# Kernel optimization log

Measured on AMD Instinct MI355X. Metric: run time of the kernel, lower is better.

Reference implementation:

```python
import jax, jax.numpy as jnp
import numpy as np

HEADS = 8
CPH = 32


def _rel_pos_indices(h, w):
    # same construction as the torch buffer, done statically in numpy
    coords = np.stack(np.meshgrid(np.arange(h), np.arange(w), indexing='ij')).reshape(2, -1)  # [2, N]
    rel = coords[:, :, None] - coords[:, None, :]  # [2, N, N]
    idx = (rel[0] + h - 1) * (2 * w - 1) + (rel[1] + w - 1)  # [N, N]
    return jnp.asarray(idx, dtype=jnp.int32)


def setup_inputs() -> dict:
    key = jax.random.key(0)
    ks = jax.random.split(key, 6)
    B, C, H, W = 2, 256, 48, 48
    emb = HEADS * CPH  # 256
    x = jax.random.normal(ks[0], (B, C, H, W), dtype=jnp.float32)
    # GDN params (kept positive so sqrt is well-defined)
    gdn_beta = jnp.ones((C,), dtype=jnp.float32)
    gdn_gamma = 0.1 * jnp.eye(C, dtype=jnp.float32) + 0.001 * jax.random.uniform(ks[1], (C, C), dtype=jnp.float32)
    w_qkv = 0.02 * jax.random.normal(ks[2], (3 * emb, C), dtype=jnp.float32)
    w_out = 0.02 * jax.random.normal(ks[3], (C, emb), dtype=jnp.float32)
    b_out = jnp.zeros((C,), dtype=jnp.float32)
    table_size = (2 * H - 1) * (2 * W - 1)
    rel_bias_table = 0.02 * jax.random.normal(ks[4], (table_size, HEADS), dtype=jnp.float32)
    return {"x": x, "gdn_beta": gdn_beta, "gdn_gamma": gdn_gamma,
            "w_qkv": w_qkv, "w_out": w_out, "b_out": b_out,
            "rel_bias_table": rel_bias_table}


def reference(x, gdn_beta, gdn_gamma, w_qkv, w_out, b_out, rel_bias_table):
    B, C, H, W = x.shape
    N = H * W
    emb = HEADS * CPH
    scale = CPH ** (-0.5)

    # GDN: y = x / sqrt(beta + gamma * x^2)  (1x1 conv over channels of x^2)
    norm = jnp.einsum('bchw,dc->bdhw', x * x, gdn_gamma) + gdn_beta[None, :, None, None]
    xn = x / jnp.sqrt(norm)

    # flatten spatial, channels last: [B, N, C]
    t = xn.reshape(B, C, N).transpose(0, 2, 1)

    # qkv projection (no bias)
    qkv = (t @ w_qkv.T).reshape(B, N, 3, HEADS, CPH).transpose(2, 0, 3, 1, 4)  # [3, B, h, N, d]
    q, k, v = qkv[0], qkv[1], qkv[2]

    attn = jnp.einsum('bhnd,bhmd->bhnm', q, k) * scale  # [B, h, N, N]

    # gathered relative position bias: [h, N, N]
    idx = _rel_pos_indices(H, W)  # [N, N], static ints
    bias = rel_bias_table[idx.reshape(-1)].reshape(N, N, HEADS).transpose(2, 0, 1)
    attn = jax.nn.softmax(attn + bias[None], axis=-1)

    # NOTE: faithful to the original quirk — reshape (B, h, N, d) directly
    # to (B, N, C) with NO head/seq transpose, exactly like the torch code.
    res = jnp.einsum('bhnm,bhmd->bhnd', attn, v).reshape(B, N, emb)

    out = res @ w_out.T + b_out  # [B, N, C]
    return out.transpose(0, 2, 1).reshape(B, C, H, W)
```

## Files before the change

kernel.cpp:

```cpp
#include <hip/hip_runtime.h>
#include <cstdint>
#include <cstddef>

typedef __attribute__((ext_vector_type(8))) short short8;
typedef __attribute__((ext_vector_type(4))) float floatx4;

#define NB 2
#define NPIX 2304
#define TBL 9025
#define TBLP 9032
#define L2E 1.4426950408889634f
#define QSCALE 0.17677669529663689f
#define NTILES 36

__device__ __forceinline__ float b2f(unsigned short u) {
  union { unsigned int i; float f; } v; v.i = ((unsigned int)u) << 16; return v.f;
}
__device__ __forceinline__ unsigned short f2b(float f) {
  union { float f; unsigned int i; } v; v.f = f;
  return (unsigned short)((v.i + 0x7fffu + ((v.i >> 16) & 1u)) >> 16);
}
__device__ __forceinline__ unsigned int cvtpk(float lo, float hi) {
  unsigned int r;
  asm("v_cvt_pk_bf16_f32 %0, %1, %2" : "=v"(r) : "v"(lo), "v"(hi));
  return r;
}

__global__ __launch_bounds__(256) void prep_k(
    const float* __restrict__ gamma, const float* __restrict__ wqkv,
    const float* __restrict__ wout, const float* __restrict__ table,
    const float* __restrict__ x,
    unsigned short* __restrict__ gb, unsigned short* __restrict__ qb,
    unsigned short* __restrict__ wb, unsigned short* __restrict__ tb,
    unsigned short* __restrict__ xsq)
{
  __shared__ unsigned short Ls[64][66];
  const int bx = blockIdx.x;
  const int tid = threadIdx.x;
  if (bx < 768) {
    int i = bx * 256 + tid;
    if (i < 65536)  gb[i] = f2b(gamma[i]);
    qb[i] = f2b(wqkv[i]);
    if (i < 65536)  wb[i] = f2b(wout[i]);
    if (i < TBL * 8) {
      int e = i >> 3, h = i & 7;
      tb[(size_t)h * TBLP + e] = f2b(table[i] * L2E);
    }
    return;
  }
  const int t = bx - 768;
  const int b = t / 144, r = t % 144;
  const int c0 = (r / 36) * 64, n0 = (r % 36) * 64;
  {
    const int ci = tid >> 2, ng = (tid & 3) * 16;
    const float* xr = &x[((size_t)(b * 256 + c0 + ci)) * NPIX + n0 + ng];
    unsigned int* dst = (unsigned int*)&Ls[ci][ng];
    #pragma unroll
    for (int j = 0; j < 4; ++j) {
      float4 v = *(const float4*)(xr + j * 4);
      dst[j * 2]     = cvtpk(v.x * v.x, v.y * v.y);
      dst[j * 2 + 1] = cvtpk(v.z * v.z, v.w * v.w);
    }
  }
  __syncthreads();
  {
    const int nr = tid >> 2, cc = (tid & 3) * 16;
    unsigned short* orow = &xsq[((size_t)(b * NPIX) + n0 + nr) * 256 + c0 + cc];
    unsigned short tmp[16];
    #pragma unroll
    for (int j = 0; j < 16; ++j) tmp[j] = Ls[cc + j][nr];
    *(short8*)&orow[0] = *(short8*)&tmp[0];
    *(short8*)&orow[8] = *(short8*)&tmp[8];
  }
}

template<int MODE>
__global__ __launch_bounds__(256) void gemm_k(
    const unsigned short* __restrict__ A,
    const unsigned short* __restrict__ Bw,
    const float* __restrict__ vec,
    const float* __restrict__ X,
    unsigned short* __restrict__ o0,
    unsigned short* __restrict__ o1,
    unsigned short* __restrict__ o2,
    float* __restrict__ of)
{
  const int n0 = blockIdx.x * 64;
  const int m0 = blockIdx.y * 64;
  const int b  = blockIdx.z;
  const int tid = threadIdx.x;
  const int wave = tid >> 6, lane = tid & 63;
  const int wm = wave >> 1, wn = wave & 1;
  const int lm = lane & 15, quad = lane >> 4;

  const unsigned short* pa = &A[(size_t)(m0 + wm * 32 + lm) * 256 + quad * 8];
  const unsigned short* pb = &Bw[((size_t)b * NPIX + n0 + wn * 32 + lm) * 256 + quad * 8];

  floatx4 acc[2][2] = {};
  #pragma unroll
  for (int k0 = 0; k0 < 256; k0 += 32) {
    short8 af0 = *(const short8*)(pa + k0);
    short8 af1 = *(const short8*)(pa + 16 * 256 + k0);
    short8 bf0 = *(const short8*)(pb + k0);
    short8 bf1 = *(const short8*)(pb + 16 * 256 + k0);
    acc[0][0] = __builtin_amdgcn_mfma_f32_16x16x32_bf16(af0, bf0, acc[0][0], 0, 0, 0);
    acc[0][1] = __builtin_amdgcn_mfma_f32_16x16x32_bf16(af0, bf1, acc[0][1], 0, 0, 0);
    acc[1][0] = __builtin_amdgcn_mfma_f32_16x16x32_bf16(af1, bf0, acc[1][0], 0, 0, 0);
    acc[1][1] = __builtin_amdgcn_mfma_f32_16x16x32_bf16(af1, bf1, acc[1][1], 0, 0, 0);
  }

  #pragma unroll
  for (int tm = 0; tm < 2; ++tm) {
    const int rbase = m0 + wm * 32 + tm * 16 + quad * 4;
    #pragma unroll
    for (int tn = 0; tn < 2; ++tn) {
      const int col = n0 + wn * 32 + tn * 16 + lm;
      floatx4 a4 = acc[tm][tn];
      if (MODE == 0) {
        float xn[4];
        #pragma unroll
        for (int r = 0; r < 4; ++r) {
          int d = rbase + r;
          float xv = X[((size_t)(b * 256 + d)) * NPIX + col];
          xn[r] = xv * rsqrtf(vec[d] + a4[r]);
        }
        uint2 pk = { cvtpk(xn[0], xn[1]), cvtpk(xn[2], xn[3]) };
        *(uint2*)&o0[((size_t)(b * NPIX + col)) * 256 + rbase] = pk;
      } else if (MODE == 1) {
        const int part = rbase >> 8, h = (rbase >> 5) & 7, dd = rbase & 31;
        if (part == 2) {
          #pragma unroll
          for (int r = 0; r < 4; ++r)
            o2[(((size_t)(b * 8 + h)) * 32 + dd + r) * NPIX + col] = f2b(a4[r]);
        } else {
          unsigned short* dst = part == 0 ? o0 : o1;
          const float sc = (part == 0) ? (QSCALE * L2E) : 1.0f;
          uint2 pk = { cvtpk(a4[0] * sc, a4[1] * sc), cvtpk(a4[2] * sc, a4[3] * sc) };
          *(uint2*)&dst[(((size_t)(b * 8 + h)) * NPIX + col) * 32 + dd] = pk;
        }
      } else {
        #pragma unroll
        for (int r = 0; r < 4; ++r) {
          int c = rbase + r;
          of[((size_t)(b * 256 + c)) * NPIX + col] = a4[r] + vec[c];
        }
      }
    }
  }
}

__global__ __launch_bounds__(576) void attn_k(
    const unsigned short* __restrict__ qg, const unsigned short* __restrict__ kg,
    const unsigned short* __restrict__ vt, const unsigned short* __restrict__ tabt,
    unsigned short* __restrict__ ob)
{
  __shared__ __align__(16) unsigned short tab[TBLP];
  __shared__ __align__(16) unsigned short Pl[9][16][72];

  const int tid = threadIdx.x;
  const int w = tid >> 6, lane = tid & 63;
  const int lm = lane & 15, quad = lane >> 4;
  const int bh = blockIdx.x;
  const int q0 = blockIdx.y * 144;
  const size_t base = (size_t)bh * NPIX * 32;

  {
    const unsigned short* src = tabt + (size_t)(bh & 7) * TBLP;
    for (int e = tid * 8; e < TBLP; e += 4608)
      *(short8*)&tab[e] = *(const short8*)&src[e];
  }
  __syncthreads();

  const int q = q0 + w * 16 + lm;
  const short8 qfrag = *(const short8*)&qg[base + (size_t)q * 32 + quad * 8];

  const int hi = (q * 43691) >> 21;
  const int rb = (hi + 47) * 95 + (q - hi * 48) + 47;

  float lsum = 0.f;
  floatx4 o[2] = {};

  for (int t = 0; t < NTILES; ++t) {
    const int j0 = t * 64;
    floatx4 s4[4];
    #pragma unroll
    for (int kt = 0; kt < 4; ++kt) {
      short8 kf = *(const short8*)&kg[base + (size_t)(j0 + kt * 16 + lm) * 32 + quad * 8];
      floatx4 z = {};
      s4[kt] = __builtin_amdgcn_mfma_f32_16x16x32_bf16(kf, qfrag, z, 0, 0, 0);
    }
    #pragma unroll
    for (int kt = 0; kt < 4; ++kt) {
      const int kk = j0 + kt * 16 + quad * 4;
      const int hj = (kk * 43691) >> 21;
      const int bb = rb - kk - hj * 47;
      float pv[4];
      #pragma unroll
      for (int r = 0; r < 4; ++r) {
        float p = exp2f(s4[kt][r] + b2f(tab[bb - r]));
        lsum += p;
        pv[r] = p;
      }
      uint2 pk = { cvtpk(pv[0], pv[1]), cvtpk(pv[2], pv[3]) };
      *(uint2*)&Pl[w][lm][kt * 16 + quad * 4] = pk;
    }
    __asm__ volatile("s_waitcnt lgkmcnt(0)" ::: "memory");
    #pragma unroll
    for (int c = 0; c < 2; ++c) {
      short8 pf = *(const short8*)&Pl[w][lm][c * 32 + quad * 8];
      #pragma unroll
      for (int dt = 0; dt < 2; ++dt) {
        short8 vf = *(const short8*)&vt[base + (size_t)(dt * 16 + lm) * NPIX + j0 + c * 32 + quad * 8];
        o[dt] = __builtin_amdgcn_mfma_f32_16x16x32_bf16(vf, pf, o[dt], 0, 0, 0);
      }
    }
  }

  lsum += __shfl_xor(lsum, 16, 64);
  lsum += __shfl_xor(lsum, 32, 64);
  const float inv = 1.f / lsum;

  #pragma unroll
  for (int dt = 0; dt < 2; ++dt) {
    uint2 pk = { cvtpk(o[dt][0] * inv, o[dt][1] * inv),
                 cvtpk(o[dt][2] * inv, o[dt][3] * inv) };
    *(uint2*)&ob[base + (size_t)q * 32 + dt * 16 + quad * 4] = pk;
  }
}

extern "C" void kernel_launch(void* const* d_in, const int* in_sizes, int n_in,
                              void* d_out, int out_size, void* d_ws, size_t ws_size,
                              hipStream_t stream) {
  const float* x     = (const float*)d_in[0];
  const float* beta  = (const float*)d_in[1];
  const float* gamma = (const float*)d_in[2];
  const float* wqkv  = (const float*)d_in[3];
  const float* wout  = (const float*)d_in[4];
  const float* bout  = (const float*)d_in[5];
  const float* table = (const float*)d_in[6];
  float* out = (float*)d_out;

  unsigned short* ws = (unsigned short*)d_ws;
  const size_t NE = (size_t)NB * NPIX * 256;
  unsigned short* xn_t  = ws;
  unsigned short* qbuf  = ws + NE;
  unsigned short* kbuf  = ws + 2 * NE;
  unsigned short* vtbuf = ws + 3 * NE;
  unsigned short* obuf  = ws + 4 * NE;
  unsigned short* gam_b = obuf;
  unsigned short* qkv_b = obuf + 65536;
  unsigned short* out_b = ws + 5 * NE;
  unsigned short* tab_t = ws + 5 * NE + 65536;
  unsigned short* xsq   = qbuf;

  prep_k<<<1056, 256, 0, stream>>>(gamma, wqkv, wout, table, x,
                                   gam_b, qkv_b, out_b, tab_t, xsq);
  gemm_k<0><<<dim3(36, 4, 2), 256, 0, stream>>>(gam_b, xsq, beta, x,
                                                xn_t, nullptr, nullptr, nullptr);
  gemm_k<1><<<dim3(36, 12, 2), 256, 0, stream>>>(qkv_b, xn_t, nullptr, nullptr,
                                                 qbuf, kbuf, vtbuf, nullptr);
  attn_k<<<dim3(16, 16), 576, 0, stream>>>(qbuf, kbuf, vtbuf, tab_t, obuf);
  gemm_k<2><<<dim3(36, 4, 2), 256, 0, stream>>>(out_b, obuf, bout, nullptr,
                                                nullptr, nullptr, nullptr, out);
}
```

Measured before the change: 167.1 us.

## Remove prep kernel by fusing fp32-to-bf16 conversions into consumer kernels

Drops the separate prep kernel that converted weights, the bias table and x² to bf16. The GDN GEMM now loads fp32 gamma and x, squares and transposes through LDS, and the QKV and output GEMMs convert fp32 weights in registers. The attention kernel gathers and scales its per-head bias table straight from the fp32 table. This removes one launch and the intermediate bf16 buffers, at the cost of doubled weight-load bandwidth, redundant per-block conversions, and a strided table gather in every attention block.

```diff
diff --git a/kernel.cpp b/kernel.cpp
--- a/kernel.cpp
+++ b/kernel.cpp
@@ -25,61 +25,94 @@
   asm("v_cvt_pk_bf16_f32 %0, %1, %2" : "=v"(r) : "v"(lo), "v"(hi));
   return r;
 }
-
-__global__ __launch_bounds__(256) void prep_k(
-    const float* __restrict__ gamma, const float* __restrict__ wqkv,
-    const float* __restrict__ wout, const float* __restrict__ table,
-    const float* __restrict__ x,
-    unsigned short* __restrict__ gb, unsigned short* __restrict__ qb,
-    unsigned short* __restrict__ wb, unsigned short* __restrict__ tb,
-    unsigned short* __restrict__ xsq)
+__device__ __forceinline__ short8 cvt8(float4 a, float4 b) {
+  union { short8 s; unsigned int u[4]; } w;
+  w.u[0] = cvtpk(a.x, a.y); w.u[1] = cvtpk(a.z, a.w);
+  w.u[2] = cvtpk(b.x, b.y); w.u[3] = cvtpk(b.z, b.w);
+  return w.s;
+}
+
+__global__ __launch_bounds__(256) void gemm0_k(
+    const float* __restrict__ Afp,
+    const float* __restrict__ X,
+    const float* __restrict__ vec,
+    unsigned short* __restrict__ o0)
 {
-  __shared__ unsigned short Ls[64][66];
-  const int bx = blockIdx.x;
+  __shared__ unsigned short Al[64][40];
+  __shared__ unsigned short Bl[64][40];
+  const int n0 = blockIdx.x * 64;
+  const int m0 = blockIdx.y * 64;
+  const int b  = blockIdx.z;
   const int tid = threadIdx.x;
-  if (bx < 768) {
-    int i = bx * 256 + tid;
-    if (i < 65536)  gb[i] = f2b(gamma[i]);
-    qb[i] = f2b(wqkv[i]);
-    if (i < 65536)  wb[i] = f2b(wout[i]);
-    if (i < TBL * 8) {
-      int e = i >> 3, h = i & 7;
-      tb[(size_t)h * TBLP + e] = f2b(table[i] * L2E);
-    }
-    return;
-  }
-  const int t = bx - 768;
-  const int b = t / 144, r = t % 144;
-  const int c0 = (r / 36) * 64, n0 = (r % 36) * 64;
-  {
-    const int ci = tid >> 2, ng = (tid & 3) * 16;
-    const float* xr = &x[((size_t)(b * 256 + c0 + ci)) * NPIX + n0 + ng];
-    unsigned int* dst = (unsigned int*)&Ls[ci][ng];
-    #pragma unroll
-    for (int j = 0; j < 4; ++j) {
-      float4 v = *(const float4*)(xr + j * 4);
-      dst[j * 2]     = cvtpk(v.x * v.x, v.y * v.y);
-      dst[j * 2 + 1] = cvtpk(v.z * v.z, v.w * v.w);
-    }
-  }
-  __syncthreads();
-  {
-    const int nr = tid >> 2, cc = (tid & 3) * 16;
-    unsigned short* orow = &xsq[((size_t)(b * NPIX) + n0 + nr) * 256 + c0 + cc];
-    unsigned short tmp[16];
-    #pragma unroll
-    for (int j = 0; j < 16; ++j) tmp[j] = Ls[cc + j][nr];
-    *(short8*)&orow[0] = *(short8*)&tmp[0];
-    *(short8*)&orow[8] = *(short8*)&tmp[8];
+  const int wave = tid >> 6, lane = tid & 63;
+  const int wm = wave >> 1, wn = wave & 1;
+  const int lm = lane & 15, quad = lane >> 4;
+
+  floatx4 acc[2][2] = {};
+
+  for (int k0 = 0; k0 < 256; k0 += 32) {
+    __syncthreads();
+    {
+      int ml = tid >> 2, ko = (tid & 3) * 8;
+      const float* ar = &Afp[(size_t)(m0 + ml) * 256 + k0 + ko];
+      float4 a0 = *(const float4*)ar;
+      float4 a1 = *(const float4*)(ar + 4);
+      *(short8*)&Al[ml][ko] = cvt8(a0, a1);
+    }
+    {
+      int kk = tid >> 3, n8 = (tid & 7) * 8;
+      const float* xr = &X[((size_t)(b * 256 + k0 + kk)) * NPIX + n0 + n8];
+      float4 x0 = *(const float4*)xr;
+      float4 x1 = *(const float4*)(xr + 4);
+      Bl[n8 + 0][kk] = f2b(x0.x * x0.x);
+      Bl[n8 + 1][kk] = f2b(x0.y * x0.y);
+      Bl[n8 + 2][kk] = f2b(x0.z * x0.z);
+      Bl[n8 + 3][kk] = f2b(x0.w * x0.w);
+      Bl[n8 + 4][kk] = f2b(x1.x * x1.x);
+      Bl[n8 + 5][kk] = f2b(x1.y * x1.y);
+      Bl[n8 + 6][kk] = f2b(x1.z * x1.z);
+      Bl[n8 + 7][kk] = f2b(x1.w * x1.w);
+    }
+    __syncthreads();
+    short8 af[2], bfr[2];
+    #pragma unroll
+    for (int tm = 0; tm < 2; ++tm)
+      af[tm] = *(const short8*)&Al[wm * 32 + tm * 16 + lm][quad * 8];
+    #pragma unroll
+    for (int tn = 0; tn < 2; ++tn)
+      bfr[tn] = *(const short8*)&Bl[wn * 32 + tn * 16 + lm][quad * 8];
+    #pragma unroll
+    for (int tm = 0; tm < 2; ++tm)
+      #pragma unroll
+      for (int tn = 0; tn < 2; ++tn)
+        acc[tm][tn] = __builtin_amdgcn_mfma_f32_16x16x32_bf16(af[tm], bfr[tn], acc[tm][tn], 0, 0, 0);
+  }
+
+  #pragma unroll
+  for (int tm = 0; tm < 2; ++tm) {
+    const int rbase = m0 + wm * 32 + tm * 16 + quad * 4;
+    #pragma unroll
+    for (int tn = 0; tn < 2; ++tn) {
+      const int col = n0 + wn * 32 + tn * 16 + lm;
+      floatx4 a4 = acc[tm][tn];
+      float xn[4];
+      #pragma unroll
+      for (int r = 0; r < 4; ++r) {
+        int d = rbase + r;
+        float xv = X[((size_t)(b * 256 + d)) * NPIX + col];
+        xn[r] = xv * rsqrtf(vec[d] + a4[r]);
+      }
+      uint2 pk = { cvtpk(xn[0], xn[1]), cvtpk(xn[2], xn[3]) };
+      *(uint2*)&o0[((size_t)(b * NPIX + col)) * 256 + rbase] = pk;
+    }
   }
 }
 
 template<int MODE>
 __global__ __launch_bounds__(256) void gemm_k(
-    const unsigned short* __restrict__ A,
+    const float* __restrict__ A,
     const unsigned short* __restrict__ Bw,
     const float* __restrict__ vec,
-    const float* __restrict__ X,
     unsigned short* __restrict__ o0,
     unsigned short* __restrict__ o1,
     unsigned short* __restrict__ o2,
@@ -93,14 +126,18 @@
   const int wm = wave >> 1, wn = wave & 1;
   const int lm = lane & 15, quad = lane >> 4;
 
-  const unsigned short* pa = &A[(size_t)(m0 + wm * 32 + lm) * 256 + quad * 8];
+  const float* pa = &A[(size_t)(m0 + wm * 32 + lm) * 256 + quad * 8];
   const unsigned short* pb = &Bw[((size_t)b * NPIX + n0 + wn * 32 + lm) * 256 + quad * 8];
 
   floatx4 acc[2][2] = {};
   #pragma unroll
   for (int k0 = 0; k0 < 256; k0 += 32) {
-    short8 af0 = *(const short8*)(pa + k0);
-    short8 af1 = *(const short8*)(pa + 16 * 256 + k0);
+    float4 a00 = *(const float4*)(pa + k0);
+    float4 a01 = *(const float4*)(pa + k0 + 4);
+    float4 a10 = *(const float4*)(pa + 16 * 256 + k0);
+    float4 a11 = *(const float4*)(pa + 16 * 256 + k0 + 4);
+    short8 af0 = cvt8(a00, a01);
+    short8 af1 = cvt8(a10, a11);
     short8 bf0 = *(const short8*)(pb + k0);
     short8 bf1 = *(const short8*)(pb + 16 * 256 + k0);
     acc[0][0] = __builtin_amdgcn_mfma_f32_16x16x32_bf16(af0, bf0, acc[0][0], 0, 0, 0);
@@ -116,17 +153,7 @@
     for (int tn = 0; tn < 2; ++tn) {
       const int col = n0 + wn * 32 + tn * 16 + lm;
       floatx4 a4 = acc[tm][tn];
-      if (MODE == 0) {
-        float xn[4];
-        #pragma unroll
-        for (int r = 0; r < 4; ++r) {
-          int d = rbase + r;
-          float xv = X[((size_t)(b * 256 + d)) * NPIX + col];
-          xn[r] = xv * rsqrtf(vec[d] + a4[r]);
-        }
-        uint2 pk = { cvtpk(xn[0], xn[1]), cvtpk(xn[2], xn[3]) };
-        *(uint2*)&o0[((size_t)(b * NPIX + col)) * 256 + rbase] = pk;
-      } else if (MODE == 1) {
+      if (MODE == 1) {
         const int part = rbase >> 8, h = (rbase >> 5) & 7, dd = rbase & 31;
         if (part == 2) {
           #pragma unroll
@@ -151,7 +178,7 @@
 
 __global__ __launch_bounds__(576) void attn_k(
     const unsigned short* __restrict__ qg, const unsigned short* __restrict__ kg,
-    const unsigned short* __restrict__ vt, const unsigned short* __restrict__ tabt,
+    const unsigned short* __restrict__ vt, const float* __restrict__ table,
     unsigned short* __restrict__ ob)
 {
   __shared__ __align__(16) unsigned short tab[TBLP];
@@ -163,11 +190,19 @@
   const int bh = blockIdx.x;
   const int q0 = blockIdx.y * 144;
   const size_t base = (size_t)bh * NPIX * 32;
+  const int h8 = bh & 7;
 
   {
-    const unsigned short* src = tabt + (size_t)(bh & 7) * TBLP;
-    for (int e = tid * 8; e < TBLP; e += 4608)
-      *(short8*)&tab[e] = *(const short8*)&src[e];
+    for (int e0 = tid * 8; e0 < TBLP; e0 += 4608) {
+      union { short8 s; unsigned short us[8]; } wv;
+      #pragma unroll
+      for (int j = 0; j < 8; ++j) {
+        const int e = e0 + j;
+        const float v = (e < TBL) ? table[(size_t)e * 8 + h8] * L2E : 0.f;
+        wv.us[j] = f2b(v);
+      }
+      *(short8*)&tab[e0] = wv.s;
+    }
   }
   __syncthreads();
 
@@ -247,19 +282,11 @@
   unsigned short* kbuf  = ws + 2 * NE;
   unsigned short* vtbuf = ws + 3 * NE;
   unsigned short* obuf  = ws + 4 * NE;
-  unsigned short* gam_b = obuf;
-  unsigned short* qkv_b = obuf + 65536;
-  unsigned short* out_b = ws + 5 * NE;
-  unsigned short* tab_t = ws + 5 * NE + 65536;
-  unsigned short* xsq   = qbuf;
-
-  prep_k<<<1056, 256, 0, stream>>>(gamma, wqkv, wout, table, x,
-                                   gam_b, qkv_b, out_b, tab_t, xsq);
-  gemm_k<0><<<dim3(36, 4, 2), 256, 0, stream>>>(gam_b, xsq, beta, x,
-                                                xn_t, nullptr, nullptr, nullptr);
-  gemm_k<1><<<dim3(36, 12, 2), 256, 0, stream>>>(qkv_b, xn_t, nullptr, nullptr,
+
+  gemm0_k<<<dim3(36, 4, 2), 256, 0, stream>>>(gamma, x, beta, xn_t);
+  gemm_k<1><<<dim3(36, 12, 2), 256, 0, stream>>>(wqkv, xn_t, nullptr,
                                                  qbuf, kbuf, vtbuf, nullptr);
-  attn_k<<<dim3(16, 16), 576, 0, stream>>>(qbuf, kbuf, vtbuf, tab_t, obuf);
-  gemm_k<2><<<dim3(36, 4, 2), 256, 0, stream>>>(out_b, obuf, bout, nullptr,
-                                                nullptr, nullptr, nullptr, out);
-}
+  attn_k<<<dim3(16, 16), 576, 0, stream>>>(qbuf, kbuf, vtbuf, table, obuf);
+  gemm_k<2><<<dim3(36, 4, 2), 256, 0, stream>>>(wout, obuf, bout, nullptr,
+                                                nullptr, nullptr, out);
+}
```

Result: slower. 182.4 us (+9.2%).

## Fuse x-squared transpose into GDN GEMM and stage GEMM tiles through LDS

Applied to the files above, without the earlier changes.

Drops the x^2 transpose/convert stage from the prep kernel. The GDN GEMM now reads fp32 x directly, squares it, converts it to bf16 and writes it transposed into shared memory, which removes a global round trip of the xsq buffer. All GEMM modes now load A and B tiles cooperatively into LDS, with two barriers per K step, instead of each wave loading fragments straight from global memory. Packing also switches from the hardware cvt_pk instruction to a software f2b rounding. The scalar transposed LDS stores in mode 0 may cause bank conflicts, and the GEMMs are small, so the barriers may add latency.

```diff
diff --git a/kernel.cpp b/kernel.cpp
--- a/kernel.cpp
+++ b/kernel.cpp
@@ -4,6 +4,7 @@
 
 typedef __attribute__((ext_vector_type(8))) short short8;
 typedef __attribute__((ext_vector_type(4))) float floatx4;
+typedef __attribute__((ext_vector_type(4))) unsigned short ushort4v;
 
 #define NB 2
 #define NPIX 2304
@@ -29,62 +30,34 @@
 __global__ __launch_bounds__(256) void prep_k(
     const float* __restrict__ gamma, const float* __restrict__ wqkv,
     const float* __restrict__ wout, const float* __restrict__ table,
-    const float* __restrict__ x,
     unsigned short* __restrict__ gb, unsigned short* __restrict__ qb,
-    unsigned short* __restrict__ wb, unsigned short* __restrict__ tb,
-    unsigned short* __restrict__ xsq)
+    unsigned short* __restrict__ wb, unsigned short* __restrict__ tb)
 {
-  __shared__ unsigned short Ls[64][66];
-  const int bx = blockIdx.x;
-  const int tid = threadIdx.x;
-  if (bx < 768) {
-    int i = bx * 256 + tid;
-    if (i < 65536)  gb[i] = f2b(gamma[i]);
-    qb[i] = f2b(wqkv[i]);
-    if (i < 65536)  wb[i] = f2b(wout[i]);
-    if (i < TBL * 8) {
-      int e = i >> 3, h = i & 7;
-      tb[(size_t)h * TBLP + e] = f2b(table[i] * L2E);
-    }
-    return;
-  }
-  const int t = bx - 768;
-  const int b = t / 144, r = t % 144;
-  const int c0 = (r / 36) * 64, n0 = (r % 36) * 64;
-  {
-    const int ci = tid >> 2, ng = (tid & 3) * 16;
-    const float* xr = &x[((size_t)(b * 256 + c0 + ci)) * NPIX + n0 + ng];
-    unsigned int* dst = (unsigned int*)&Ls[ci][ng];
-    #pragma unroll
-    for (int j = 0; j < 4; ++j) {
-      float4 v = *(const float4*)(xr + j * 4);
-      dst[j * 2]     = cvtpk(v.x * v.x, v.y * v.y);
-      dst[j * 2 + 1] = cvtpk(v.z * v.z, v.w * v.w);
-    }
-  }
-  __syncthreads();
-  {
-    const int nr = tid >> 2, cc = (tid & 3) * 16;
-    unsigned short* orow = &xsq[((size_t)(b * NPIX) + n0 + nr) * 256 + c0 + cc];
-    unsigned short tmp[16];
-    #pragma unroll
-    for (int j = 0; j < 16; ++j) tmp[j] = Ls[cc + j][nr];
-    *(short8*)&orow[0] = *(short8*)&tmp[0];
-    *(short8*)&orow[8] = *(short8*)&tmp[8];
+  int i = blockIdx.x * 256 + threadIdx.x;
+  if (i < 65536)  gb[i] = f2b(gamma[i]);
+  if (i < 196608) qb[i] = f2b(wqkv[i]);
+  if (i < 65536)  wb[i] = f2b(wout[i]);
+  if (i < TBL * 8) {
+    int e = i >> 3, h = i & 7;
+    tb[(size_t)h * TBLP + e] = f2b(table[i] * L2E);
   }
 }
 
 template<int MODE>
 __global__ __launch_bounds__(256) void gemm_k(
     const unsigned short* __restrict__ A,
-    const unsigned short* __restrict__ Bw,
+    const void* __restrict__ Bv,
     const float* __restrict__ vec,
-    const float* __restrict__ X,
     unsigned short* __restrict__ o0,
     unsigned short* __restrict__ o1,
     unsigned short* __restrict__ o2,
     float* __restrict__ of)
 {
+  __shared__ unsigned short Al[64][40];
+  __shared__ unsigned short Bl[64][40];
+  const float* __restrict__ X = (const float*)Bv;
+  const unsigned short* __restrict__ Bw = (const unsigned short*)Bv;
+
   const int n0 = blockIdx.x * 64;
   const int m0 = blockIdx.y * 64;
   const int b  = blockIdx.z;
@@ -93,39 +66,63 @@
   const int wm = wave >> 1, wn = wave & 1;
   const int lm = lane & 15, quad = lane >> 4;
 
-  const unsigned short* pa = &A[(size_t)(m0 + wm * 32 + lm) * 256 + quad * 8];
-  const unsigned short* pb = &Bw[((size_t)b * NPIX + n0 + wn * 32 + lm) * 256 + quad * 8];
-
   floatx4 acc[2][2] = {};
-  #pragma unroll
+
   for (int k0 = 0; k0 < 256; k0 += 32) {
-    short8 af0 = *(const short8*)(pa + k0);
-    short8 af1 = *(const short8*)(pa + 16 * 256 + k0);
-    short8 bf0 = *(const short8*)(pb + k0);
-    short8 bf1 = *(const short8*)(pb + 16 * 256 + k0);
-    acc[0][0] = __builtin_amdgcn_mfma_f32_16x16x32_bf16(af0, bf0, acc[0][0], 0, 0, 0);
-    acc[0][1] = __builtin_amdgcn_mfma_f32_16x16x32_bf16(af0, bf1, acc[0][1], 0, 0, 0);
-    acc[1][0] = __builtin_amdgcn_mfma_f32_16x16x32_bf16(af1, bf0, acc[1][0], 0, 0, 0);
-    acc[1][1] = __builtin_amdgcn_mfma_f32_16x16x32_bf16(af1, bf1, acc[1][1], 0, 0, 0);
+    __syncthreads();
+    {
+      int ml = tid >> 2, ko = (tid & 3) * 8;
+      *(short8*)&Al[ml][ko] = *(const short8*)&A[(size_t)(m0 + ml) * 256 + k0 + ko];
+    }
+    if (MODE == 0) {
+      int kk = tid >> 3, n8 = (tid & 7) * 8;
+      const float* xr = &X[((size_t)(b * 256 + k0 + kk)) * NPIX + n0 + n8];
+      float4 x0 = *(const float4*)xr;
+      float4 x1 = *(const float4*)(xr + 4);
+      Bl[n8 + 0][kk] = f2b(x0.x * x0.x);
+      Bl[n8 + 1][kk] = f2b(x0.y * x0.y);
+      Bl[n8 + 2][kk] = f2b(x0.z * x0.z);
+      Bl[n8 + 3][kk] = f2b(x0.w * x0.w);
+      Bl[n8 + 4][kk] = f2b(x1.x * x1.x);
+      Bl[n8 + 5][kk] = f2b(x1.y * x1.y);
+      Bl[n8 + 6][kk] = f2b(x1.z * x1.z);
+      Bl[n8 + 7][kk] = f2b(x1.w * x1.w);
+    } else {
+      int nl = tid >> 2, ko = (tid & 3) * 8;
+      short8 bv = *(const short8*)&Bw[((size_t)b * NPIX + n0 + nl) * 256 + k0 + ko];
+      *(short8*)&Bl[nl][ko] = bv;
+    }
+    __syncthreads();
+    short8 af[2], bfr[2];
+    #pragma unroll
+    for (int tm = 0; tm < 2; ++tm)
+      af[tm] = *(const short8*)&Al[wm*32 + tm*16 + lm][quad*8];
+    #pragma unroll
+    for (int tn = 0; tn < 2; ++tn)
+      bfr[tn] = *(const short8*)&Bl[wn*32 + tn*16 + lm][quad*8];
+    #pragma unroll
+    for (int tm = 0; tm < 2; ++tm)
+      #pragma unroll
+      for (int tn = 0; tn < 2; ++tn)
+        acc[tm][tn] = __builtin_amdgcn_mfma_f32_16x16x32_bf16(af[tm], bfr[tn], acc[tm][tn], 0, 0, 0);
   }
 
   #pragma unroll
   for (int tm = 0; tm < 2; ++tm) {
-    const int rbase = m0 + wm * 32 + tm * 16 + quad * 4;
+    const int rbase = m0 + wm*32 + tm*16 + quad*4;
     #pragma unroll
     for (int tn = 0; tn < 2; ++tn) {
-      const int col = n0 + wn * 32 + tn * 16 + lm;
+      const int col = n0 + wn*32 + tn*16 + lm;
       floatx4 a4 = acc[tm][tn];
       if (MODE == 0) {
-        float xn[4];
+        ushort4v pk;
         #pragma unroll
         for (int r = 0; r < 4; ++r) {
           int d = rbase + r;
           float xv = X[((size_t)(b * 256 + d)) * NPIX + col];
-          xn[r] = xv * rsqrtf(vec[d] + a4[r]);
+          pk[r] = f2b(xv * rsqrtf(vec[d] + a4[r]));
         }
-        uint2 pk = { cvtpk(xn[0], xn[1]), cvtpk(xn[2], xn[3]) };
-        *(uint2*)&o0[((size_t)(b * NPIX + col)) * 256 + rbase] = pk;
+        *(ushort4v*)&o0[((size_t)(b * NPIX + col)) * 256 + rbase] = pk;
       } else if (MODE == 1) {
         const int part = rbase >> 8, h = (rbase >> 5) & 7, dd = rbase & 31;
         if (part == 2) {
@@ -135,8 +132,10 @@
         } else {
           unsigned short* dst = part == 0 ? o0 : o1;
           const float sc = (part == 0) ? (QSCALE * L2E) : 1.0f;
-          uint2 pk = { cvtpk(a4[0] * sc, a4[1] * sc), cvtpk(a4[2] * sc, a4[3] * sc) };
-          *(uint2*)&dst[(((size_t)(b * 8 + h)) * NPIX + col) * 32 + dd] = pk;
+          ushort4v pk;
+          #pragma unroll
+          for (int r = 0; r < 4; ++r) pk[r] = f2b(a4[r] * sc);
+          *(ushort4v*)&dst[(((size_t)(b * 8 + h)) * NPIX + col) * 32 + dd] = pk;
         }
       } else {
         #pragma unroll
@@ -251,15 +250,10 @@
   unsigned short* qkv_b = obuf + 65536;
   unsigned short* out_b = ws + 5 * NE;
   unsigned short* tab_t = ws + 5 * NE + 65536;
-  unsigned short* xsq   = qbuf;
-
-  prep_k<<<1056, 256, 0, stream>>>(gamma, wqkv, wout, table, x,
-                                   gam_b, qkv_b, out_b, tab_t, xsq);
-  gemm_k<0><<<dim3(36, 4, 2), 256, 0, stream>>>(gam_b, xsq, beta, x,
-                                                xn_t, nullptr, nullptr, nullptr);
-  gemm_k<1><<<dim3(36, 12, 2), 256, 0, stream>>>(qkv_b, xn_t, nullptr, nullptr,
-                                                 qbuf, kbuf, vtbuf, nullptr);
+
+  prep_k<<<768, 256, 0, stream>>>(gamma, wqkv, wout, table, gam_b, qkv_b, out_b, tab_t);
+  gemm_k<0><<<dim3(36, 4, 2), 256, 0, stream>>>(gam_b, x, beta, xn_t, nullptr, nullptr, nullptr);
+  gemm_k<1><<<dim3(36, 12, 2), 256, 0, stream>>>(qkv_b, xn_t, nullptr, qbuf, kbuf, vtbuf, nullptr);
   attn_k<<<dim3(16, 16), 576, 0, stream>>>(qbuf, kbuf, vtbuf, tab_t, obuf);
-  gemm_k<2><<<dim3(36, 4, 2), 256, 0, stream>>>(out_b, obuf, bout, nullptr,
-                                                nullptr, nullptr, nullptr, out);
-}
+  gemm_k<2><<<dim3(36, 4, 2), 256, 0, stream>>>(out_b, obuf, bout, nullptr, nullptr, nullptr, out);
+}
```

Measured after the change: 153.2 us. 1.09x faster.
